# Kernel tuning notes

Hardware: AMD Instinct MI355X
Metric: run time of the kernel (lower is better)

Reference implementation:

```python
import jax, jax.numpy as jnp
import numpy as np

B, N, D_MODEL, N_HEADS, WINDOW = 2, 2048, 1024, 16, 512
HEAD_DIM = D_MODEL // N_HEADS

def setup_inputs() -> dict:
    key = jax.random.key(0)
    k1, k2, k3 = jax.random.split(key, 3)
    x = jax.random.normal(k1, (B, N, D_MODEL), dtype=jnp.float32)
    W_qkv = jax.random.normal(k2, (D_MODEL, 3 * D_MODEL), dtype=jnp.float32) * 0.02
    W_proj = jax.random.normal(k3, (D_MODEL, D_MODEL), dtype=jnp.float32) * 0.02
    b_proj = jnp.zeros((D_MODEL,), dtype=jnp.float32)
    return {"x": x, "W_qkv": W_qkv, "W_proj": W_proj, "b_proj": b_proj}

def reference(x, W_qkv, W_proj, b_proj):
    Bx, Nx, C = x.shape
    H, Dh = N_HEADS, C // N_HEADS
    scale = Dh ** -0.5
    window = min(WINDOW, Nx)
    half = window // 2
    # qkv: [B,N,3C] -> [3,B,H,N,Dh]
    qkv = (x @ W_qkv).reshape(Bx, Nx, 3, H, Dh).transpose(2, 0, 3, 1, 4)
    q, k, v = qkv[0], qkv[1], qkv[2]
    # banded mask: allowed iff i-half <= j <= i+half
    i = jnp.arange(Nx)[:, None]
    j = jnp.arange(Nx)[None, :]
    allowed = jnp.abs(i - j) <= half  # [N,N] bool
    attn = jnp.einsum('bhqd,bhkd->bhqk', q, k) * scale
    attn = jnp.where(allowed[None, None], attn, -jnp.inf)
    attn = jax.nn.softmax(attn, axis=-1)
    out = jnp.einsum('bhqk,bhkd->bhqd', attn, v)
    out = out.transpose(0, 2, 1, 3).reshape(Bx, Nx, C)
    return out @ W_proj + b_proj
```

## Files before the change

### kernel.cpp

```cpp
#include <hip/hip_runtime.h>
#include <stdint.h>


typedef _Float16 f16x8 __attribute__((ext_vector_type(8)));
typedef _Float16 f16x4 __attribute__((ext_vector_type(4)));
typedef float    f32x4 __attribute__((ext_vector_type(4)));
typedef float    f32x16 __attribute__((ext_vector_type(16)));

#define MFMA16(a, b, c) __builtin_amdgcn_mfma_f32_16x16x32_f16((a), (b), (c), 0, 0, 0)
#define MFMA32(a, b, c) __builtin_amdgcn_mfma_f32_32x32x16_f16((a), (b), (c), 0, 0, 0)

__device__ __forceinline__ void gload16(const void* g, void* l) {
  __builtin_amdgcn_global_load_lds(
      (const __attribute__((address_space(1))) void*)g,
      (__attribute__((address_space(3))) void*)l, 16, 0, 0);
}

__global__ __launch_bounds__(256) void prep(const float* __restrict__ x,
                                            const float* __restrict__ wqkv,
                                            const float* __restrict__ wproj,
                                            _Float16* __restrict__ Xb,
                                            _Float16* __restrict__ Wqt,
                                            _Float16* __restrict__ Wpt) {
  __shared__ float t[64][65];
  const int id = blockIdx.x, tid = threadIdx.x;
  if (id < 4096) {
    int i = (id * 256 + tid) * 4;
    float4 v = *(const float4*)(x + i);
    f16x4 h;
    h[0] = (_Float16)v.x; h[1] = (_Float16)v.y;
    h[2] = (_Float16)v.z; h[3] = (_Float16)v.w;
    *(f16x4*)(Xb + i) = h;
    return;
  }
  const float* in; _Float16* out; int N, bx, by;
  if (id < 4864) { int tt = id - 4096; in = wqkv; out = Wqt; N = 3072; bx = tt % 48; by = tt / 48; }
  else           { int tt = id - 4864; in = wproj; out = Wpt; N = 1024; bx = tt & 15; by = tt >> 4; }
  const int n0 = bx * 64, k0 = by * 64;
  {
    int j = tid & 63;
#pragma unroll
    for (int p = 0; p < 16; p++) {
      int i = p * 4 + (tid >> 6);
      t[i][j] = in[(size_t)(k0 + i) * N + n0 + j];
    }
  }
  __syncthreads();
  {
    int i = tid & 63;
#pragma unroll
    for (int p = 0; p < 16; p++) {
      int j = p * 4 + (tid >> 6);
      out[(size_t)(n0 + j) * 1024 + k0 + i] = (_Float16)t[i][j];
    }
  }
}

__global__ __launch_bounds__(256) void vtrans(const _Float16* __restrict__ V,
                                              _Float16* __restrict__ Vt) {
  __shared__ _Float16 t[64][66];
  const int tid = threadIdx.x;
  const int bh = blockIdx.y, n0 = blockIdx.x * 64;
  const _Float16* Vg = V + (size_t)bh * 131072;
  {
    int dh0 = (tid & 7) * 8;
#pragma unroll
    for (int p = 0; p < 2; p++) {
      int nl = p * 32 + (tid >> 3);
      f16x8 v = *(const f16x8*)(Vg + (size_t)(n0 + nl) * 64 + dh0);
#pragma unroll
      for (int e = 0; e < 8; e++) t[nl][dh0 + e] = v[e];
    }
  }
  __syncthreads();
  {
    int dh = tid >> 2, nb = (tid & 3) * 16;
    f16x8 a, b;
#pragma unroll
    for (int e = 0; e < 8; e++) { a[e] = t[nb + e][dh]; b[e] = t[nb + 8 + e][dh]; }
    _Float16* dst = Vt + (size_t)bh * 131072 + (size_t)dh * 2048 + n0 + nb;
    *(f16x8*)dst = a;
    *(f16x8*)(dst + 8) = b;
  }
}

template <int BM, int BN, int EPI>
__global__ __launch_bounds__(256) void gemm16(const _Float16* __restrict__ A,
                                              const _Float16* __restrict__ Bt,
                                              const int K,
                                              _Float16* __restrict__ oh,
                                              float* __restrict__ of,
                                              const float* __restrict__ bias,
                                              const int Nout) {
  constexpr int RF = BM / 32, CF = BN / 32;
  constexpr int SLABS = (BM + BN) / 8;
  __shared__ __align__(16) char smem[(BM + BN) * 128];
  char* As = smem;
  char* Bs = smem + BM * 128;
  const int tid = threadIdx.x, wave = tid >> 6, lane = tid & 63;
  const int il = lane & 15, ih = lane >> 4;
  const int bm = blockIdx.y * BM, bn = blockIdx.x * BN;
  const int wm = wave >> 1, wn = wave & 1;
  const int rs = lane >> 3, cp = lane & 7;

  f32x4 acc[RF][CF] = {};

  for (int k0 = 0; k0 < K; k0 += 64) {
    __syncthreads();
#pragma unroll
    for (int s0 = 0; s0 < SLABS / 4; s0++) {
      int s = wave + s0 * 4;
      int row = s * 8 + rs;
      int c = cp ^ (row & 7);
      if (row < BM)
        gload16(A + (size_t)(bm + row) * K + k0 + c * 8, As + s * 1024);
      else
        gload16(Bt + (size_t)(bn + row - BM) * K + k0 + c * 8, smem + s * 1024);
    }
    __syncthreads();
#pragma unroll
    for (int ks = 0; ks < 2; ks++) {
      f16x8 af[RF], bf[CF];
#pragma unroll
      for (int rf = 0; rf < RF; rf++) {
        int R = wm * (BM / 2) + rf * 16 + il;
        af[rf] = *(const f16x8*)(As + R * 128 + (((ks * 4 + ih) ^ (R & 7)) * 16));
      }
#pragma unroll
      for (int cf = 0; cf < CF; cf++) {
        int C = wn * (BN / 2) + cf * 16 + il;
        bf[cf] = *(const f16x8*)(Bs + C * 128 + (((ks * 4 + ih) ^ (C & 7)) * 16));
      }
#pragma unroll
      for (int rf = 0; rf < RF; rf++)
#pragma unroll
        for (int cf = 0; cf < CF; cf++)
          acc[rf][cf] = MFMA16(af[rf], bf[cf], acc[rf][cf]);
    }
  }

#pragma unroll
  for (int rf = 0; rf < RF; rf++)
#pragma unroll
    for (int cf = 0; cf < CF; cf++)
#pragma unroll
      for (int r = 0; r < 4; r++) {
        int row = bm + wm * (BM / 2) + rf * 16 + ih * 4 + r;
        int col = bn + wn * (BN / 2) + cf * 16 + il;
        float v = acc[rf][cf][r];
        if (EPI == 0) {
          int sec = col >> 10, cc = col & 1023;
          if (sec == 0) v *= 0.18033688f;
          size_t plane = (size_t)(sec * 32 + (row >> 11) * 16 + (cc >> 6));
          oh[plane * 131072 + (size_t)(row & 2047) * 64 + (cc & 63)] = (_Float16)v;
        } else {
          of[(size_t)row * Nout + col] = v + bias[col];
        }
      }
}

__global__ __launch_bounds__(512) void attn(const _Float16* __restrict__ QKV,
                                            const _Float16* __restrict__ VT,
                                            _Float16* __restrict__ O2) {
  __shared__ __align__(16) char smem[65536];
  char* Ks = smem + 32768;
  char* Vs = smem + 49152;
  const int tid = threadIdx.x, wave = tid >> 6, lane = tid & 63;
  const int qw = wave >> 1, sh = wave & 1;
  const int cl = lane & 31, hl = lane >> 5;
  const int rs = lane >> 3, cp = lane & 7;
  const int q0 = blockIdx.x * 128, bh = blockIdx.y;
  const _Float16* Qg = QKV + (size_t)bh * 131072;
  const _Float16* Kg = QKV + 4194304 + (size_t)bh * 131072;
  const _Float16* Vg = VT + (size_t)bh * 131072;
  const int t0 = (q0 >= 256) ? q0 - 256 : 0;
  const int t1 = (q0 + 384 <= 2048) ? q0 + 384 : 2048;
  const int niter = (t1 - t0) >> 7;

#pragma unroll
  for (int q = 0; q < 2; q++) {
    int s = 2 * wave + q;
    int row = s * 8 + rs;
    int c = cp ^ (row & 7);
    gload16(Qg + (size_t)(q0 + row) * 64 + c * 8, smem + s * 1024);
  }
#pragma unroll
  for (int q = 0; q < 2; q++) {
    int s = 2 * wave + q;
    int krow = s * 8 + rs;
    int c = cp ^ (krow & 7);
    gload16(Kg + (size_t)(t0 + krow) * 64 + c * 8, Ks + s * 1024);
    int sub = s >> 3, vrow = (s & 7) * 8 + rs;
    int cv = cp ^ (vrow & 7);
    gload16(Vg + (size_t)vrow * 2048 + t0 + 64 * sub + cv * 8,
            Vs + sub * 8192 + (s & 7) * 1024);
  }
  __syncthreads();
  f16x8 bq[4];
  {
    int row = 32 * qw + cl;
#pragma unroll
    for (int ks = 0; ks < 4; ks++)
      bq[ks] = *(const f16x8*)(smem + row * 128 + (((ks * 2 + hl) ^ (row & 7)) * 16));
  }
  __syncthreads();

  char* Pw = smem + wave * 4096;
  f32x16 oacc[2] = {};
  float l_acc = 0.f;
  const int a0 = q0 + 32 * qw;

  for (int i = 0; i < niter; i++) {
    const int kt = t0 + i * 128;
    const int d0a = a0 - (kt + 64 * sh);
    const int d0b = d0a - 32;
    const bool deadA = (d0a >= 288) || (d0a <= -288);
    const bool deadB = (d0b >= 288) || (d0b <= -288);
    if (!(deadA && deadB)) {
#pragma unroll
      for (int cb = 0; cb < 2; cb++) {
        const int d0 = cb ? d0b : d0a;
        const bool dead = cb ? deadB : deadA;
        if (dead) {
#pragma unroll
          for (int g = 0; g < 4; g++) {
            f16x4 z = {};
            *(f16x4*)(Pw + cl * 128 + (((4 * cb + g) ^ (cl & 7)) * 16) + 8 * hl) = z;
          }
          continue;
        }
        f32x16 st = {};
        const int krow = 64 * sh + 32 * cb + cl;
#pragma unroll
        for (int ks = 0; ks < 4; ks++) {
          f16x8 ak = *(const f16x8*)(Ks + krow * 128 + (((ks * 2 + hl) ^ (krow & 7)) * 16));
          st = MFMA32(ak, bq[ks], st);
        }
#pragma unroll
        for (int g = 0; g < 4; g++) {
          f16x4 hv;
#pragma unroll
          for (int i2 = 0; i2 < 4; i2++) {
            float e = __builtin_amdgcn_exp2f(st[g * 4 + i2]);
            int rowk = 8 * g + 4 * hl + i2;
            if (d0 == 256) e = (cl <= rowk) ? e : 0.f;
            else if (d0 == -256) e = (cl >= rowk) ? e : 0.f;
            l_acc += e;
            hv[i2] = (_Float16)e;
          }
          *(f16x4*)(Pw + cl * 128 + (((4 * cb + g) ^ (cl & 7)) * 16) + 8 * hl) = hv;
        }
      }
      f16x8 bp[4];
#pragma unroll
      for (int ks = 0; ks < 4; ks++)
        bp[ks] = *(const f16x8*)(Pw + cl * 128 + (((ks * 2 + hl) ^ (cl & 7)) * 16));
#pragma unroll
      for (int db = 0; db < 2; db++) {
        const int vrow = 32 * db + cl;
#pragma unroll
        for (int ks = 0; ks < 4; ks++) {
          f16x8 av = *(const f16x8*)(Vs + sh * 8192 + vrow * 128 +
                                     (((ks * 2 + hl) ^ (vrow & 7)) * 16));
          oacc[db] = MFMA32(av, bp[ks], oacc[db]);
        }
      }
    }
    __syncthreads();
    if (i + 1 < niter) {
      const int kt2 = kt + 128;
#pragma unroll
      for (int q = 0; q < 2; q++) {
        int s = 2 * wave + q;
        int krow = s * 8 + rs;
        int c = cp ^ (krow & 7);
        gload16(Kg + (size_t)(kt2 + krow) * 64 + c * 8, Ks + s * 1024);
        int sub = s >> 3, vrow = (s & 7) * 8 + rs;
        int cv = cp ^ (vrow & 7);
        gload16(Vg + (size_t)vrow * 2048 + kt2 + 64 * sub + cv * 8,
                Vs + sub * 8192 + (s & 7) * 1024);
      }
    }
    __syncthreads();
  }

  l_acc += __shfl_xor(l_acc, 32);
  float* ov = (float*)oacc;
  if (sh == 1) {
#pragma unroll
    for (int r = 0; r < 8; r++)
      *(f32x4*)(smem + qw * 8192 + lane * 128 + r * 16) = *(const f32x4*)(ov + r * 4);
    *(float*)(smem + 32768 + qw * 128 + cl * 4) = l_acc;
  }
  __syncthreads();
  if (sh == 0) {
    float inv = 1.0f / (l_acc + *(const float*)(smem + 32768 + qw * 128 + cl * 4));
    const int b = bh >> 4, h = bh & 15;
    _Float16* dst = O2 + (size_t)(b * 2048 + q0 + 32 * qw + cl) * 1024 + h * 64;
#pragma unroll
    for (int db = 0; db < 2; db++)
#pragma unroll
      for (int g = 0; g < 4; g++) {
        f32x4 po = *(const f32x4*)(smem + qw * 8192 + lane * 128 + (db * 4 + g) * 16);
        f16x4 hv;
#pragma unroll
        for (int i2 = 0; i2 < 4; i2++)
          hv[i2] = (_Float16)((ov[db * 16 + g * 4 + i2] + po[i2]) * inv);
        *(f16x4*)(dst + 32 * db + 8 * g + 4 * hl) = hv;
      }
  }
}


extern "C" void kernel_launch(void* const* d_in, const int* in_sizes, int n_in,
                              void* d_out, int out_size, void* d_ws, size_t ws_size,
                              hipStream_t stream) {
  const float* x = (const float*)d_in[0];
  const float* wqkv = (const float*)d_in[1];
  const float* wproj = (const float*)d_in[2];
  const float* bproj = (const float*)d_in[3];
  float* out = (float*)d_out;
  char* ws = (char*)d_ws;

  _Float16* Xb  = (_Float16*)(ws);
  _Float16* Wqt = (_Float16*)(ws + (size_t)(8  << 20));
  _Float16* Wpt = (_Float16*)(ws + (size_t)(14 << 20));
  _Float16* QKV = (_Float16*)(ws + (size_t)(16 << 20));
  _Float16* Vt  = (_Float16*)(ws + (size_t)(40 << 20));
  _Float16* O2  = (_Float16*)(ws);

  prep<<<5120, 256, 0, stream>>>(x, wqkv, wproj, Xb, Wqt, Wpt);
  gemm16<128, 128, 0><<<dim3(24, 32), 256, 0, stream>>>(Xb, Wqt, 1024, QKV, nullptr,
                                                        nullptr, 0);
  vtrans<<<dim3(32, 32), 256, 0, stream>>>(QKV + 8388608, Vt);
  attn<<<dim3(16, 32), 512, 0, stream>>>(QKV, Vt, O2);
  gemm16<128, 64, 1><<<dim3(16, 32), 256, 0, stream>>>(O2, Wpt, 1024, nullptr, out,
                                                       bproj, 1024);
}
```

Baseline: 167.2 us.

## Restructure attention kernel: 256-query blocks, register P, double-buffered K/V

Each attention block now covers 256 queries, one 32-query strip per wave, instead of 128 queries split over key halves, so the cross-wave output merge goes away. P is kept in registers via packed fp16 conversion and lane shuffles rather than a round trip through LDS. K/V tiles are 64 keys and double-buffered, with the next tile's loads issued before compute, leaving one barrier per iteration. The grid halves to 256 blocks, which lowers occupancy and parallelism on a large GPU.

New measurement: 175.1 us. 4.7% more time.

```diff
diff --git a/kernel.cpp b/kernel.cpp
--- a/kernel.cpp
+++ b/kernel.cpp
@@ -4,6 +4,7 @@
 
 typedef _Float16 f16x8 __attribute__((ext_vector_type(8)));
 typedef _Float16 f16x4 __attribute__((ext_vector_type(4)));
+typedef __fp16   fp16x2n __attribute__((ext_vector_type(2)));
 typedef float    f32x4 __attribute__((ext_vector_type(4)));
 typedef float    f32x16 __attribute__((ext_vector_type(16)));
 
@@ -14,6 +15,11 @@
   __builtin_amdgcn_global_load_lds(
       (const __attribute__((address_space(1))) void*)g,
       (__attribute__((address_space(3))) void*)l, 16, 0, 0);
+}
+
+__device__ __forceinline__ unsigned pk2(float a, float b) {
+  fp16x2n t = __builtin_amdgcn_cvt_pkrtz(a, b);
+  return __builtin_bit_cast(unsigned, t);
 }
 
 __global__ __launch_bounds__(256) void prep(const float* __restrict__ x,
@@ -163,152 +169,120 @@
                                             const _Float16* __restrict__ VT,
                                             _Float16* __restrict__ O2) {
   __shared__ __align__(16) char smem[65536];
-  char* Ks = smem + 32768;
-  char* Vs = smem + 49152;
+  char* Qs = smem;
   const int tid = threadIdx.x, wave = tid >> 6, lane = tid & 63;
-  const int qw = wave >> 1, sh = wave & 1;
   const int cl = lane & 31, hl = lane >> 5;
   const int rs = lane >> 3, cp = lane & 7;
-  const int q0 = blockIdx.x * 128, bh = blockIdx.y;
+  const int q0 = blockIdx.x * 256, bh = blockIdx.y;
   const _Float16* Qg = QKV + (size_t)bh * 131072;
   const _Float16* Kg = QKV + 4194304 + (size_t)bh * 131072;
   const _Float16* Vg = VT + (size_t)bh * 131072;
   const int t0 = (q0 >= 256) ? q0 - 256 : 0;
-  const int t1 = (q0 + 384 <= 2048) ? q0 + 384 : 2048;
-  const int niter = (t1 - t0) >> 7;
-
-#pragma unroll
-  for (int q = 0; q < 2; q++) {
-    int s = 2 * wave + q;
+  const int t1 = (q0 + 512 <= 2048) ? q0 + 512 : 2048;
+  const int niter = (t1 - t0) >> 6;
+
+#pragma unroll
+  for (int s0 = 0; s0 < 4; s0++) {
+    int s = wave * 4 + s0;
     int row = s * 8 + rs;
     int c = cp ^ (row & 7);
-    gload16(Qg + (size_t)(q0 + row) * 64 + c * 8, smem + s * 1024);
-  }
-#pragma unroll
-  for (int q = 0; q < 2; q++) {
-    int s = 2 * wave + q;
-    int krow = s * 8 + rs;
-    int c = cp ^ (krow & 7);
-    gload16(Kg + (size_t)(t0 + krow) * 64 + c * 8, Ks + s * 1024);
-    int sub = s >> 3, vrow = (s & 7) * 8 + rs;
-    int cv = cp ^ (vrow & 7);
-    gload16(Vg + (size_t)vrow * 2048 + t0 + 64 * sub + cv * 8,
-            Vs + sub * 8192 + (s & 7) * 1024);
+    gload16(Qg + (size_t)(q0 + row) * 64 + c * 8, Qs + s * 1024);
+  }
+  {
+    char* B0 = smem + 32768;
+    int row = wave * 8 + rs;
+    int c = cp ^ (row & 7);
+    gload16(Kg + (size_t)(t0 + row) * 64 + c * 8, B0 + wave * 1024);
+    gload16(Vg + (size_t)row * 2048 + t0 + c * 8, B0 + 8192 + wave * 1024);
   }
   __syncthreads();
+
   f16x8 bq[4];
   {
-    int row = 32 * qw + cl;
+    int row = 32 * wave + cl;
 #pragma unroll
     for (int ks = 0; ks < 4; ks++)
-      bq[ks] = *(const f16x8*)(smem + row * 128 + (((ks * 2 + hl) ^ (row & 7)) * 16));
-  }
-  __syncthreads();
-
-  char* Pw = smem + wave * 4096;
+      bq[ks] = *(const f16x8*)(Qs + row * 128 + (((ks * 2 + hl) ^ (row & 7)) * 16));
+  }
+
   f32x16 oacc[2] = {};
   float l_acc = 0.f;
-  const int a0 = q0 + 32 * qw;
+  const int a0 = q0 + 32 * wave;
 
   for (int i = 0; i < niter; i++) {
-    const int kt = t0 + i * 128;
-    const int d0a = a0 - (kt + 64 * sh);
-    const int d0b = d0a - 32;
-    const bool deadA = (d0a >= 288) || (d0a <= -288);
-    const bool deadB = (d0b >= 288) || (d0b <= -288);
-    if (!(deadA && deadB)) {
-#pragma unroll
-      for (int cb = 0; cb < 2; cb++) {
-        const int d0 = cb ? d0b : d0a;
-        const bool dead = cb ? deadB : deadA;
-        if (dead) {
-#pragma unroll
-          for (int g = 0; g < 4; g++) {
-            f16x4 z = {};
-            *(f16x4*)(Pw + cl * 128 + (((4 * cb + g) ^ (cl & 7)) * 16) + 8 * hl) = z;
-          }
-          continue;
+    const int kt = t0 + i * 64;
+    char* Bc = smem + 32768 + (i & 1) * 16384;
+    if (i + 1 < niter) {
+      char* Bn = smem + 32768 + ((i + 1) & 1) * 16384;
+      int row = wave * 8 + rs;
+      int c = cp ^ (row & 7);
+      gload16(Kg + (size_t)(kt + 64 + row) * 64 + c * 8, Bn + wave * 1024);
+      gload16(Vg + (size_t)row * 2048 + (kt + 64) + c * 8, Bn + 8192 + wave * 1024);
+    }
+    char* Ksm = Bc;
+    char* Vsm = Bc + 8192;
+#pragma unroll
+    for (int cb = 0; cb < 2; cb++) {
+      const int d0 = a0 - (kt + 32 * cb);
+      if (d0 >= 288 || d0 <= -288) continue;
+      f32x16 st = {};
+#pragma unroll
+      for (int ks = 0; ks < 4; ks++) {
+        int krow = 32 * cb + cl;
+        f16x8 ak = *(const f16x8*)(Ksm + krow * 128 + (((ks * 2 + hl) ^ (krow & 7)) * 16));
+        st = MFMA32(ak, bq[ks], st);
+      }
+      uint32_t q4x[4], q4y[4];
+#pragma unroll
+      for (int g = 0; g < 4; g++) {
+        float v[4];
+#pragma unroll
+        for (int i2 = 0; i2 < 4; i2++) {
+          float e = __builtin_amdgcn_exp2f(st[4 * g + i2]);
+          int kl = 8 * g + 4 * hl + i2;
+          if (d0 == 256) e = (cl <= kl) ? e : 0.f;
+          else if (d0 == -256) e = (cl >= kl) ? e : 0.f;
+          l_acc += e;
+          v[i2] = e;
         }
-        f32x16 st = {};
-        const int krow = 64 * sh + 32 * cb + cl;
-#pragma unroll
-        for (int ks = 0; ks < 4; ks++) {
-          f16x8 ak = *(const f16x8*)(Ks + krow * 128 + (((ks * 2 + hl) ^ (krow & 7)) * 16));
-          st = MFMA32(ak, bq[ks], st);
+        q4x[g] = pk2(v[0], v[1]);
+        q4y[g] = pk2(v[2], v[3]);
+      }
+#pragma unroll
+      for (int ks2 = 0; ks2 < 2; ks2++) {
+        uint32_t qax = q4x[2 * ks2], qay = q4y[2 * ks2];
+        uint32_t qbx = q4x[2 * ks2 + 1], qby = q4y[2 * ks2 + 1];
+        uint32_t rax = __shfl_xor(qax, 32), ray = __shfl_xor(qay, 32);
+        uint32_t rbx = __shfl_xor(qbx, 32), rby = __shfl_xor(qby, 32);
+        uint32_t lox = hl ? rbx : qax, loy = hl ? rby : qay;
+        uint32_t hix = hl ? qbx : rax, hiy = hl ? qby : ray;
+        union { uint32_t u[4]; f16x8 h; } bp;
+        bp.u[0] = lox; bp.u[1] = loy; bp.u[2] = hix; bp.u[3] = hiy;
+#pragma unroll
+        for (int db = 0; db < 2; db++) {
+          int vrow = 32 * db + cl;
+          f16x8 av = *(const f16x8*)(Vsm + vrow * 128 +
+                                     (((cb * 4 + ks2 * 2 + hl) ^ (vrow & 7)) * 16));
+          oacc[db] = MFMA32(av, bp.h, oacc[db]);
         }
-#pragma unroll
-        for (int g = 0; g < 4; g++) {
-          f16x4 hv;
-#pragma unroll
-          for (int i2 = 0; i2 < 4; i2++) {
-            float e = __builtin_amdgcn_exp2f(st[g * 4 + i2]);
-            int rowk = 8 * g + 4 * hl + i2;
-            if (d0 == 256) e = (cl <= rowk) ? e : 0.f;
-            else if (d0 == -256) e = (cl >= rowk) ? e : 0.f;
-            l_acc += e;
-            hv[i2] = (_Float16)e;
-          }
-          *(f16x4*)(Pw + cl * 128 + (((4 * cb + g) ^ (cl & 7)) * 16) + 8 * hl) = hv;
-        }
-      }
-      f16x8 bp[4];
-#pragma unroll
-      for (int ks = 0; ks < 4; ks++)
-        bp[ks] = *(const f16x8*)(Pw + cl * 128 + (((ks * 2 + hl) ^ (cl & 7)) * 16));
-#pragma unroll
-      for (int db = 0; db < 2; db++) {
-        const int vrow = 32 * db + cl;
-#pragma unroll
-        for (int ks = 0; ks < 4; ks++) {
-          f16x8 av = *(const f16x8*)(Vs + sh * 8192 + vrow * 128 +
-                                     (((ks * 2 + hl) ^ (vrow & 7)) * 16));
-          oacc[db] = MFMA32(av, bp[ks], oacc[db]);
-        }
       }
     }
     __syncthreads();
-    if (i + 1 < niter) {
-      const int kt2 = kt + 128;
-#pragma unroll
-      for (int q = 0; q < 2; q++) {
-        int s = 2 * wave + q;
-        int krow = s * 8 + rs;
-        int c = cp ^ (krow & 7);
-        gload16(Kg + (size_t)(kt2 + krow) * 64 + c * 8, Ks + s * 1024);
-        int sub = s >> 3, vrow = (s & 7) * 8 + rs;
-        int cv = cp ^ (vrow & 7);
-        gload16(Vg + (size_t)vrow * 2048 + kt2 + 64 * sub + cv * 8,
-                Vs + sub * 8192 + (s & 7) * 1024);
-      }
-    }
-    __syncthreads();
   }
 
   l_acc += __shfl_xor(l_acc, 32);
-  float* ov = (float*)oacc;
-  if (sh == 1) {
-#pragma unroll
-    for (int r = 0; r < 8; r++)
-      *(f32x4*)(smem + qw * 8192 + lane * 128 + r * 16) = *(const f32x4*)(ov + r * 4);
-    *(float*)(smem + 32768 + qw * 128 + cl * 4) = l_acc;
-  }
-  __syncthreads();
-  if (sh == 0) {
-    float inv = 1.0f / (l_acc + *(const float*)(smem + 32768 + qw * 128 + cl * 4));
-    const int b = bh >> 4, h = bh & 15;
-    _Float16* dst = O2 + (size_t)(b * 2048 + q0 + 32 * qw + cl) * 1024 + h * 64;
-#pragma unroll
-    for (int db = 0; db < 2; db++)
-#pragma unroll
-      for (int g = 0; g < 4; g++) {
-        f32x4 po = *(const f32x4*)(smem + qw * 8192 + lane * 128 + (db * 4 + g) * 16);
-        f16x4 hv;
-#pragma unroll
-        for (int i2 = 0; i2 < 4; i2++)
-          hv[i2] = (_Float16)((ov[db * 16 + g * 4 + i2] + po[i2]) * inv);
-        *(f16x4*)(dst + 32 * db + 8 * g + 4 * hl) = hv;
-      }
-  }
+  const float inv = 1.0f / l_acc;
+  const int b = bh >> 4, h = bh & 15;
+  _Float16* dst = O2 + (size_t)(b * 2048 + a0 + cl) * 1024 + h * 64;
+#pragma unroll
+  for (int db = 0; db < 2; db++)
+#pragma unroll
+    for (int g = 0; g < 4; g++) {
+      uint32_t lo = pk2(oacc[db][4 * g + 0] * inv, oacc[db][4 * g + 1] * inv);
+      uint32_t hi = pk2(oacc[db][4 * g + 2] * inv, oacc[db][4 * g + 3] * inv);
+      uint2 pkd = {lo, hi};
+      *(uint2*)(dst + 32 * db + 8 * g + 4 * hl) = pkd;
+    }
 }
 
 
@@ -333,7 +307,7 @@
   gemm16<128, 128, 0><<<dim3(24, 32), 256, 0, stream>>>(Xb, Wqt, 1024, QKV, nullptr,
                                                         nullptr, 0);
   vtrans<<<dim3(32, 32), 256, 0, stream>>>(QKV + 8388608, Vt);
-  attn<<<dim3(16, 32), 512, 0, stream>>>(QKV, Vt, O2);
+  attn<<<dim3(8, 32), 512, 0, stream>>>(QKV, Vt, O2);
   gemm16<128, 64, 1><<<dim3(16, 32), 256, 0, stream>>>(O2, Wpt, 1024, nullptr, out,
                                                        bproj, 1024);
 }
```
